# Performance work log

Measured on AMD Instinct MI355X. Metric: run time of the kernel, lower is better.

## Reference

```python
import jax, jax.numpy as jnp
import numpy as np

B, SQ, D = 4, 2048, 1536
HEADS, KV_HEADS, HEAD_DIM = 24, 12, 64
CROSS_DIM = 768
TEXT_LEN, NUM_TOKENS = 512, 64
ENC_LEN = TEXT_LEN + NUM_TOKENS
ROT_DIM = 32
IP_SCALE = 1.0
SCALE = 1.0 / np.sqrt(HEAD_DIM).astype(np.float32)


def _split_heads(x, n_heads):
    # [B, S, n_heads*HEAD_DIM] -> [B, n_heads, S, HEAD_DIM]
    b, s, _ = x.shape
    return x.reshape(b, s, n_heads, HEAD_DIM).transpose(0, 2, 1, 3)


def _repeat_kv(x):
    # [B, KV_HEADS, S, D] -> [B, HEADS, S, D] (repeat_interleave on head dim)
    return jnp.repeat(x, HEADS // KV_HEADS, axis=1)


def _apply_rope(x, cos, sin):
    # x: [B, H, S, ROT_DIM]; cos/sin: [S, ROT_DIM]; use_real_unbind_dim=-2 convention
    xr = x.reshape(*x.shape[:-1], 2, ROT_DIM // 2)
    x_real, x_imag = xr[..., 0, :], xr[..., 1, :]
    x_rot = jnp.concatenate([-x_imag, x_real], axis=-1)
    return x * cos[None, None] + x_rot * sin[None, None]


def _attn(q, k, v):
    scores = jnp.einsum('bhqd,bhkd->bhqk', q, k) * SCALE
    probs = jax.nn.softmax(scores.astype(jnp.float32), axis=-1).astype(q.dtype)
    return jnp.einsum('bhqk,bhkd->bhqd', probs, v)


def setup_inputs():
    key = jax.random.key(0)
    ks = jax.random.split(key, 10)
    t = jnp.arange(SQ, dtype=jnp.float32)
    freqs = 1.0 / (10000.0 ** (jnp.arange(ROT_DIM // 2, dtype=jnp.float32) / (ROT_DIM // 2)))
    ang = t[:, None] * freqs[None, :]  # [SQ, ROT_DIM//2]
    rope_cos = jnp.concatenate([jnp.cos(ang), jnp.cos(ang)], axis=-1)
    rope_sin = jnp.concatenate([jnp.sin(ang), jnp.sin(ang)], axis=-1)
    s = 0.02
    return {
        'hidden_states': jax.random.normal(ks[0], (B, SQ, D), jnp.float32),
        'encoder_hidden_states': jax.random.normal(ks[1], (B, ENC_LEN, CROSS_DIM), jnp.float32),
        'rope_cos': rope_cos,
        'rope_sin': rope_sin,
        'wq': jax.random.normal(ks[2], (D, HEADS * HEAD_DIM), jnp.float32) * s,
        'wk': jax.random.normal(ks[3], (CROSS_DIM, KV_HEADS * HEAD_DIM), jnp.float32) * s,
        'wv': jax.random.normal(ks[4], (CROSS_DIM, KV_HEADS * HEAD_DIM), jnp.float32) * s,
        'wk_ip': jax.random.normal(ks[5], (CROSS_DIM, KV_HEADS * HEAD_DIM), jnp.float32) * s,
        'wv_ip': jax.random.normal(ks[6], (CROSS_DIM, KV_HEADS * HEAD_DIM), jnp.float32) * s,
        'wo': jax.random.normal(ks[7], (HEADS * HEAD_DIM, D), jnp.float32) * s,
        'bo': jnp.zeros((D,), jnp.float32),
    }


def reference(hidden_states, encoder_hidden_states, rope_cos, rope_sin,
              wq, wk, wv, wk_ip, wv_ip, wo, bo):
    residual = hidden_states
    text = encoder_hidden_states[:, :TEXT_LEN, :]
    ip = encoder_hidden_states[:, TEXT_LEN:, :]

    q = _split_heads(hidden_states @ wq, HEADS)          # [B, H, SQ, Dh]
    k = _repeat_kv(_split_heads(text @ wk, KV_HEADS))    # [B, H, St, Dh]
    v = _repeat_kv(_split_heads(text @ wv, KV_HEADS))

    # RoPE in float32 on first ROT_DIM channels of Q only (cross-attention)
    q32 = q.astype(jnp.float32)
    q_rot = _apply_rope(q32[..., :ROT_DIM], rope_cos, rope_sin)
    q = jnp.concatenate([q_rot, q32[..., ROT_DIM:]], axis=-1).astype(hidden_states.dtype)

    out = _attn(q, k, v)                                 # [B, H, SQ, Dh]

    # IP-adapter branch
    ip_k = _repeat_kv(_split_heads(ip @ wk_ip, KV_HEADS))  # [B, H, NUM_TOKENS, Dh]
    ip_v = _repeat_kv(_split_heads(ip @ wv_ip, KV_HEADS))
    out = out + IP_SCALE * _attn(q, ip_k, ip_v)

    out = out.transpose(0, 2, 1, 3).reshape(B, SQ, HEADS * HEAD_DIM)
    out = out @ wo + bo
    return out + residual
```

## Files before the change

### kernel.cpp

```cpp
#include <hip/hip_runtime.h>
#include <hip/hip_bf16.h>

typedef __attribute__((ext_vector_type(8))) short short8;
typedef __attribute__((ext_vector_type(4))) short short4v;
typedef __attribute__((ext_vector_type(4))) float f32x4;

#define MFMA16(a, b, c) __builtin_amdgcn_mfma_f32_16x16x32_bf16(a, b, c, 0, 0, 0)
#define QK_SCALE_LOG2E 0.18033688011112042f

__device__ __forceinline__ short f2bf(float x) {
  union { float f; unsigned u; } v; v.f = x;
  unsigned u = v.u;
  u += 0x7FFFu + ((u >> 16) & 1u);
  return (short)(u >> 16);
}
__device__ __forceinline__ short f2bf_trunc(float x) {
  union { float f; unsigned u; } v; v.f = x;
  return (short)(v.u >> 16);
}

__device__ __forceinline__ void gload16(const void* g, void* l) {
  __builtin_amdgcn_global_load_lds(
      (const __attribute__((address_space(1))) unsigned int*)g,
      (__attribute__((address_space(3))) unsigned int*)l, 16, 0, 0);
}

__global__ __launch_bounds__(256) void enc_pack_kernel(
    const float* __restrict__ enc, short* __restrict__ text,
    short* __restrict__ ip) {
  int i4 = blockIdx.x * 256 + threadIdx.x;
  int i = i4 * 4;
  if (i >= 4 * 576 * 768) return;
  int c = i % 768;
  int rs = i / 768;
  int b = rs / 576, s = rs % 576;
  f32x4 v = *(const f32x4*)(enc + i);
  short4v o;
  o[0] = f2bf(v[0]); o[1] = f2bf(v[1]); o[2] = f2bf(v[2]); o[3] = f2bf(v[3]);
  if (s < 512)
    *(short4v*)(text + (size_t)(b * 512 + s) * 768 + c) = o;
  else
    *(short4v*)(ip + (size_t)(b * 64 + (s - 512)) * 768 + c) = o;
}

__global__ __launch_bounds__(256) void prep_weights_kernel(
    const float* __restrict__ wq, const float* __restrict__ wo,
    const float* __restrict__ wk, const float* __restrict__ wv,
    const float* __restrict__ wkip, const float* __restrict__ wvip,
    short* __restrict__ wqT, short* __restrict__ woT,
    short* __restrict__ wkvT, short* __restrict__ wkvipT) {
  __shared__ float tile[32][33];
  const int z = blockIdx.z;
  const float* src; short* dst; int N, row_off;
  if (z == 0)      { src = wq;   dst = wqT;    N = 1536; row_off = 0; }
  else if (z == 1) { src = wo;   dst = woT;    N = 1536; row_off = 0; }
  else if (z == 2) { src = wk;   dst = wkvT;   N = 768;  row_off = 0; }
  else if (z == 3) { src = wv;   dst = wkvT;   N = 768;  row_off = 768; }
  else if (z == 4) { src = wkip; dst = wkvipT; N = 768;  row_off = 0; }
  else             { src = wvip; dst = wkvipT; N = 768;  row_off = 768; }
  int c0 = blockIdx.x * 32, r0 = blockIdx.y * 32;
  if (c0 >= N || r0 >= N) return;
  int tx = threadIdx.x & 31, ty = threadIdx.x >> 5;
#pragma unroll
  for (int j = 0; j < 4; ++j)
    tile[ty + j * 8][tx] = src[(size_t)(r0 + ty + j * 8) * N + c0 + tx];
  __syncthreads();
#pragma unroll
  for (int j = 0; j < 4; ++j)
    dst[(size_t)(row_off + c0 + ty + j * 8) * N + r0 + tx] =
        f2bf(tile[tx][ty + j * 8]);
}

__device__ __forceinline__ void stage32(const short* __restrict__ gA,
                                        const short* __restrict__ gBt,
                                        int lda, int ldb, char* buf, int tid) {
#pragma unroll
  for (int li = 0; li < 2; ++li) {
    int L = li * 4096 + tid * 16;
    int row = L >> 6;
    int cb = (L & 63) ^ (((row >> 1) & 3) << 4);
    gload16(gA + (size_t)row * lda + (cb >> 1), buf + L);
    gload16(gBt + (size_t)row * ldb + (cb >> 1), buf + 8192 + L);
  }
}

__device__ __forceinline__ void compute32(const char* p0, int wr, int wc,
                                          int lr, int hk, int xr,
                                          f32x4 acc[4][4]) {
  short8 af[4], bf[4];
#pragma unroll
  for (int m = 0; m < 4; ++m) {
    int row = wr + m * 16 + lr;
    af[m] = *(const short8*)(p0 + row * 64 + (hk ^ xr));
  }
#pragma unroll
  for (int n = 0; n < 4; ++n) {
    int row = wc + n * 16 + lr;
    bf[n] = *(const short8*)(p0 + 8192 + row * 64 + (hk ^ xr));
  }
#pragma unroll
  for (int m = 0; m < 4; ++m)
#pragma unroll
    for (int n = 0; n < 4; ++n) acc[m][n] = MFMA16(af[m], bf[n], acc[m][n]);
}

template <int K>
__device__ __forceinline__ void gemm128p(
    const short* __restrict__ A, const short* __restrict__ Bt, int lda,
    int ldb, int row0, int col0, char* sm, f32x4 acc[4][4]) {
  const int tid = threadIdx.x;
  const int lane = tid & 63, wid = tid >> 6;
  const int wr = (wid >> 1) * 64, wc = (wid & 1) * 64;
  const int lr = lane & 15;
  const int hk = (lane >> 4) * 16;
  const int xr = ((lr >> 1) & 3) << 4;
  constexpr int NT = K / 32;

  const short* gA = A + (size_t)row0 * lda;
  const short* gB = Bt + (size_t)col0 * ldb;

  char* p0 = sm;
  char* p1 = sm + 16384;
  char* p2 = sm + 32768;

  stage32(gA, gB, lda, ldb, p0, tid);
  stage32(gA + 32, gB + 32, lda, ldb, p1, tid);
  asm volatile("s_waitcnt vmcnt(4)" ::: "memory");
  __builtin_amdgcn_s_barrier();

  for (int t = 0; t < NT; ++t) {
    if (t + 2 < NT)
      stage32(gA + (t + 2) * 32, gB + (t + 2) * 32, lda, ldb, p2, tid);
    __builtin_amdgcn_sched_barrier(0);
    compute32(p0, wr, wc, lr, hk, xr, acc);
    __builtin_amdgcn_sched_barrier(0);
    if (t + 2 < NT)
      asm volatile("s_waitcnt vmcnt(4)" ::: "memory");
    else
      asm volatile("s_waitcnt vmcnt(0)" ::: "memory");
    __builtin_amdgcn_s_barrier();
    char* tmp = p0; p0 = p1; p1 = p2; p2 = tmp;
  }
}

__device__ __forceinline__ void grid128(int& row0, int& col0) {
  int bid = blockIdx.x;
  int x = bid & 7;
  int j = bid >> 3;
  row0 = (x * 8 + (j & 7)) * 128;
  col0 = (j >> 3) * 128;
}

__device__ __forceinline__ void q_issueA(const float* __restrict__ gAf,
                                         int tid, f32x4 ar[4]) {
#pragma unroll
  for (int li = 0; li < 2; ++li) {
    int L = li * 4096 + tid * 16;
    int row = L >> 6;
    int cb = (L & 63) ^ (((row >> 1) & 3) << 4);
    const float* src = gAf + (size_t)row * 1536 + (cb >> 1);
    ar[li * 2] = *(const f32x4*)src;
    ar[li * 2 + 1] = *(const f32x4*)(src + 4);
  }
}
__device__ __forceinline__ void q_writeA(char* buf, int tid, const f32x4 ar[4]) {
#pragma unroll
  for (int li = 0; li < 2; ++li) {
    int L = li * 4096 + tid * 16;
    short8 s;
#pragma unroll
    for (int j = 0; j < 4; ++j) {
      s[j] = f2bf_trunc(ar[li * 2][j]);
      s[j + 4] = f2bf_trunc(ar[li * 2 + 1][j]);
    }
    *(short8*)(buf + L) = s;
  }
}
__device__ __forceinline__ void q_stageB(const short* __restrict__ gBt,
                                         char* buf, int tid) {
#pragma unroll
  for (int li = 0; li < 2; ++li) {
    int L = li * 4096 + tid * 16;
    int row = L >> 6;
    int cb = (L & 63) ^ (((row >> 1) & 3) << 4);
    gload16(gBt + (size_t)row * 1536 + (cb >> 1), buf + 8192 + L);
  }
}

__global__ __launch_bounds__(256, 3) void q_proj_128p(
    const float* __restrict__ hs, const short* __restrict__ wqT,
    const float* __restrict__ rc, const float* __restrict__ rsn,
    short* __restrict__ qbuf) {
  __shared__ char sm[49152];
  f32x4 acc[4][4] = {};
  int row0, col0;
  grid128(row0, col0);

  const int tid = threadIdx.x;
  const int lane = tid & 63, wid = tid >> 6;
  const int wr = (wid >> 1) * 64, wc = (wid & 1) * 64;
  const int lr = lane & 15;
  const int hk = (lane >> 4) * 16;
  const int xr = ((lr >> 1) & 3) << 4;
  constexpr int NT = 48;

  const float* gAf = hs + (size_t)row0 * 1536;
  const short* gB = wqT + (size_t)col0 * 1536;
  char* p0 = sm;
  char* p1 = sm + 16384;
  char* p2 = sm + 32768;
  f32x4 arA[4], arB[4];

  q_issueA(gAf, tid, arA);
  q_stageB(gB, p0, tid);
  q_issueA(gAf + 32, tid, arB);
  q_stageB(gB + 32, p1, tid);
  asm volatile("s_waitcnt vmcnt(8)" ::: "memory");
  q_writeA(p0, tid, arA);
  asm volatile("s_waitcnt vmcnt(6) lgkmcnt(0)" ::: "memory");
  __builtin_amdgcn_s_barrier();

  for (int t = 0; t < NT; ++t) {
    if (t + 2 < NT) {
      if ((t & 1) == 0) q_issueA(gAf + (t + 2) * 32, tid, arA);
      else              q_issueA(gAf + (t + 2) * 32, tid, arB);
      q_stageB(gB + (t + 2) * 32, p2, tid);
    }
    __builtin_amdgcn_sched_barrier(0);
    compute32(p0, wr, wc, lr, hk, xr, acc);
    __builtin_amdgcn_sched_barrier(0);
    if (t + 2 < NT)
      asm volatile("s_waitcnt vmcnt(6)" ::: "memory");
    else
      asm volatile("s_waitcnt vmcnt(0)" ::: "memory");
    if (t + 1 < NT) {
      if ((t & 1) == 0) q_writeA(p1, tid, arB);
      else              q_writeA(p1, tid, arA);
    }
    asm volatile("s_waitcnt lgkmcnt(0)" ::: "memory");
    __builtin_amdgcn_s_barrier();
    char* tmp = p0; p0 = p1; p1 = p2; p2 = tmp;
  }

  const int lrow4 = (lane >> 4) * 4;
  const int h = (col0 + wc) >> 6;
#pragma unroll
  for (int m = 0; m < 4; ++m) {
#pragma unroll
    for (int r = 0; r < 4; ++r) {
      int grow = row0 + wr + m * 16 + lrow4 + r;
      int b = grow >> 11, t = grow & 2047;
      float v0 = acc[m][0][r], v1 = acc[m][1][r];
      float c0 = rc[t * 32 + lr], s0 = rsn[t * 32 + lr];
      float c1 = rc[t * 32 + 16 + lr], s1 = rsn[t * 32 + 16 + lr];
      float n0 = (v0 * c0 - v1 * s0) * QK_SCALE_LOG2E;
      float n1 = (v1 * c1 + v0 * s1) * QK_SCALE_LOG2E;
      short* ob = qbuf + ((size_t)(b * 24 + h) * 2048 + t) * 64;
      ob[lr] = f2bf(n0);
      ob[16 + lr] = f2bf(n1);
      ob[32 + lr] = f2bf(acc[m][2][r] * QK_SCALE_LOG2E);
      ob[48 + lr] = f2bf(acc[m][3][r] * QK_SCALE_LOG2E);
    }
  }
}

__global__ __launch_bounds__(256, 3) void o_proj_128p(
    const short* __restrict__ attnbf, const short* __restrict__ woT,
    const float* __restrict__ bo, const float* __restrict__ resid,
    float* __restrict__ out) {
  __shared__ char sm[49152];
  f32x4 acc[4][4] = {};
  int row0, col0;
  grid128(row0, col0);

  const int tid = threadIdx.x;
  const int lane = tid & 63, wid = tid >> 6;
  const int wr = (wid >> 1) * 64, wc = (wid & 1) * 64;
  const int lr = lane & 15;
  const int hk = (lane >> 4) * 16;
  const int xr = ((lr >> 1) & 3) << 4;
  const int lrow4 = (lane >> 4) * 4;
  constexpr int NT = 48;

  const short* gA = attnbf + (size_t)row0 * 1536;
  const short* gB = woT + (size_t)col0 * 1536;
  char* p0 = sm;
  char* p1 = sm + 16384;
  char* p2 = sm + 32768;
  float rv[2][4][4];

  stage32(gA, gB, 1536, 1536, p0, tid);
  stage32(gA + 32, gB + 32, 1536, 1536, p1, tid);
  asm volatile("s_waitcnt vmcnt(4)" ::: "memory");
  __builtin_amdgcn_s_barrier();

  for (int t = 0; t < NT; ++t) {
    if (t + 2 < NT)
      stage32(gA + (t + 2) * 32, gB + (t + 2) * 32, 1536, 1536, p2, tid);
    if (t == NT - 2) {
#pragma unroll
      for (int m = 0; m < 2; ++m)
#pragma unroll
        for (int n = 0; n < 4; ++n)
#pragma unroll
          for (int r = 0; r < 4; ++r)
            rv[m][n][r] = resid[(size_t)(row0 + wr + m * 16 + lrow4 + r) * 1536 +
                                col0 + wc + n * 16 + lr];
    }
    __builtin_amdgcn_sched_barrier(0);
    compute32(p0, wr, wc, lr, hk, xr, acc);
    __builtin_amdgcn_sched_barrier(0);
    if (t + 2 < NT)
      asm volatile("s_waitcnt vmcnt(4)" ::: "memory");
    else if (t == NT - 2)
      asm volatile("s_waitcnt vmcnt(32)" ::: "memory");
    __builtin_amdgcn_s_barrier();
    char* tmp = p0; p0 = p1; p1 = p2; p2 = tmp;
  }

#pragma unroll
  for (int m = 0; m < 4; ++m) {
#pragma unroll
    for (int n = 0; n < 4; ++n) {
#pragma unroll
      for (int r = 0; r < 4; ++r) {
        int grow = row0 + wr + m * 16 + lrow4 + r;
        int gcol = col0 + wc + n * 16 + lr;
        size_t off = (size_t)grow * 1536 + gcol;
        float rs = (m < 2) ? rv[m & 1][n][r] : resid[off];
        out[off] = acc[m][n][r] + bo[gcol] + rs;
      }
    }
  }
}

__global__ __launch_bounds__(256, 3) void kv_gemm(
    const short* __restrict__ Abf, const short* __restrict__ wkvT,
    short* __restrict__ kout, short* __restrict__ vtout, int rlog2) {
  __shared__ char sm[49152];
  f32x4 acc[4][4] = {};
  const int row0 = blockIdx.y * 128, col0 = blockIdx.x * 128;
  gemm128p<768>(Abf, wkvT, 768, 768, row0, col0, sm, acc);

  const int tid = threadIdx.x;
  const int lane = tid & 63, wid = tid >> 6;
  const int wr = (wid >> 1) * 64, wc = (wid & 1) * 64;
  const int lr = lane & 15, lrow4 = (lane >> 4) * 4;
  const int rmask = (1 << rlog2) - 1;
#pragma unroll
  for (int m = 0; m < 4; ++m) {
#pragma unroll
    for (int n = 0; n < 4; ++n) {
#pragma unroll
      for (int r = 0; r < 4; ++r) {
        int grow = row0 + wr + m * 16 + lrow4 + r;
        int gcol = col0 + wc + n * 16 + lr;
        int b = grow >> rlog2, key = grow & rmask;
        short val = f2bf(acc[m][n][r]);
        if (gcol < 768) {
          int kvh = gcol >> 6, d = gcol & 63;
          kout[((((size_t)(b * 12 + kvh)) << rlog2) + key) * 64 + d] = val;
        } else {
          int c2 = gcol - 768;
          int kvh = c2 >> 6, d = c2 & 63;
          int kp = (key & ~31) | (((key >> 2) & 3) << 3) |
                   (((key >> 4) & 1) << 2) | (key & 3);
          vtout[(((size_t)((b * 12 + kvh) * 64 + d)) << rlog2) + kp] = val;
        }
      }
    }
  }
}

__device__ __forceinline__ void stage_tile(const short* __restrict__ ks,
                                           const short* __restrict__ vs,
                                           int vstr, short* kb, short* vb,
                                           int tid) {
#pragma unroll
  for (int q = 0; q < 2; ++q) {
    int L = q * 4096 + tid * 16;
    int row = L >> 7;
    int sc = ((L & 127) ^ ((row & 7) << 4)) >> 1;
    gload16(ks + row * 64 + sc, (char*)kb + L);
    gload16(vs + (size_t)row * vstr + sc, (char*)vb + L);
  }
}

__device__ __forceinline__ void attn_tile(const short* kb, const short* vb,
                                          const short8 qf[2],
                                          float& m_run, float& l_run,
                                          f32x4 o_acc[4], int lane) {
  const int lr = lane & 15, hi = lane >> 4;
  f32x4 s[4];
#pragma unroll
  for (int nf = 0; nf < 4; ++nf) {
    int row = nf * 16 + lr;
    int rx = (row & 7) << 4;
    const char* base = (const char*)kb + row * 128;
    short8 k0 = *(const short8*)(base + ((hi * 16) ^ rx));
    short8 k1 = *(const short8*)(base + ((64 + hi * 16) ^ rx));
    f32x4 a = {0.f, 0.f, 0.f, 0.f};
    a = MFMA16(k0, qf[0], a);
    a = MFMA16(k1, qf[1], a);
    s[nf] = a;
  }
  float mx = fmaxf(fmaxf(s[0][0], s[0][1]), fmaxf(s[0][2], s[0][3]));
#pragma unroll
  for (int nf = 1; nf < 4; ++nf)
    mx = fmaxf(mx, fmaxf(fmaxf(s[nf][0], s[nf][1]), fmaxf(s[nf][2], s[nf][3])));
  if (__any(mx - m_run > 8.0f)) {
    float mr = fmaxf(mx, __shfl_xor(mx, 16));
    mr = fmaxf(mr, __shfl_xor(mr, 32));
    float mn = fmaxf(m_run, mr);
    float corr = __builtin_amdgcn_exp2f(m_run - mn);
    m_run = mn;
    l_run *= corr;
#pragma unroll
    for (int r = 0; r < 4; ++r) {
      float cr = __shfl(corr, hi * 4 + r);
#pragma unroll
      for (int no = 0; no < 4; ++no) o_acc[no][r] *= cr;
    }
  }
  short8 pa[2];
#pragma unroll
  for (int nf = 0; nf < 4; ++nf) {
#pragma unroll
    for (int r = 0; r < 4; ++r) {
      float p = __builtin_amdgcn_exp2f(s[nf][r] - m_run);
      l_run += p;
      pa[nf >> 1][(nf & 1) * 4 + r] = f2bf_trunc(p);
    }
  }
#pragma unroll
  for (int ks = 0; ks < 2; ++ks) {
#pragma unroll
    for (int no = 0; no < 4; ++no) {
      int row = no * 16 + lr;
      int rx = (row & 7) << 4;
      short8 vf = *(const short8*)((const char*)vb + row * 128 +
                                   ((ks * 64 + hi * 16) ^ rx));
      o_acc[no] = MFMA16(pa[ks], vf, o_acc[no]);
    }
  }
}

__global__ __launch_bounds__(256, 4) void attn_kernel(
    const short* __restrict__ qbuf, const short* __restrict__ kbuf,
    const short* __restrict__ vtbuf, const short* __restrict__ kipbuf,
    const short* __restrict__ vtipbuf, short* __restrict__ attn_out) {
  const int tid = threadIdx.x;
  const int lane = tid & 63, wid = tid >> 6;
  const int f = (blockIdx.x & 7) * 384 + (blockIdx.x >> 3);
  const int qt = f & 31;
  const int h = (f >> 5) % 24;
  const int b = f / (32 * 24);
  const int kvh = h >> 1;
  const int lr = lane & 15, hi = lane >> 4;

  __shared__ short skv_k[2 * 64 * 64];
  __shared__ short skv_v[2 * 64 * 64];

  const short* qp = qbuf + (size_t)(b * 24 + h) * 2048 * 64;
  const short* kp = kbuf + (size_t)(b * 12 + kvh) * 512 * 64;
  const short* vp = vtbuf + (size_t)(b * 12 + kvh) * 64 * 512;
  const short* kip = kipbuf + (size_t)(b * 12 + kvh) * 64 * 64;
  const short* vip = vtipbuf + (size_t)(b * 12 + kvh) * 64 * 64;

  const int q0 = qt * 64 + wid * 16;
  short8 qf[2];
  qf[0] = *(const short8*)(qp + (size_t)(q0 + lr) * 64 + hi * 8);
  qf[1] = *(const short8*)(qp + (size_t)(q0 + lr) * 64 + 32 + hi * 8);

  float m1 = -1.0e30f, l1 = 0.f, m2 = -1.0e30f, l2 = 0.f;
  f32x4 oacc1[4] = {}, oacc2[4] = {};

  stage_tile(kp, vp, 512, skv_k, skv_v, tid);
  __syncthreads();

  for (int t = 0; t < 9; ++t) {
    int cur = t & 1, nxt = cur ^ 1;
    if (t < 8) {
      const short* ks_ = (t < 7) ? kp + (t + 1) * 64 * 64 : kip;
      const short* vs_ = (t < 7) ? vp + (t + 1) * 64 : vip;
      int vstr = (t < 7) ? 512 : 64;
      stage_tile(ks_, vs_, vstr, skv_k + nxt * 4096, skv_v + nxt * 4096, tid);
    }
    if (t < 8)
      attn_tile(skv_k + cur * 4096, skv_v + cur * 4096, qf, m1, l1, oacc1, lane);
    else
      attn_tile(skv_k + cur * 4096, skv_v + cur * 4096, qf, m2, l2, oacc2, lane);
    __syncthreads();
  }

  l1 += __shfl_xor(l1, 16); l1 += __shfl_xor(l1, 32);
  l2 += __shfl_xor(l2, 16); l2 += __shfl_xor(l2, 32);
  float inv1 = 1.0f / l1, inv2 = 1.0f / l2;
#pragma unroll
  for (int r = 0; r < 4; ++r) {
    float i1 = __shfl(inv1, hi * 4 + r);
    float i2 = __shfl(inv2, hi * 4 + r);
    int grow = b * 2048 + q0 + hi * 4 + r;
#pragma unroll
    for (int no = 0; no < 4; ++no) {
      float val = oacc1[no][r] * i1 + oacc2[no][r] * i2;
      attn_out[(size_t)grow * 1536 + h * 64 + no * 16 + lr] = f2bf(val);
    }
  }
}

extern "C" void kernel_launch(void* const* d_in, const int* in_sizes, int n_in,
                              void* d_out, int out_size, void* d_ws, size_t ws_size,
                              hipStream_t stream) {
  const float* hs = (const float*)d_in[0];
  const float* enc = (const float*)d_in[1];
  const float* rc = (const float*)d_in[2];
  const float* rsn = (const float*)d_in[3];
  const float* wq = (const float*)d_in[4];
  const float* wk = (const float*)d_in[5];
  const float* wv = (const float*)d_in[6];
  const float* wkip = (const float*)d_in[7];
  const float* wvip = (const float*)d_in[8];
  const float* wo = (const float*)d_in[9];
  const float* bo = (const float*)d_in[10];
  float* out = (float*)d_out;

  char* ws = (char*)d_ws;
  short* attnbuf = (short*)(ws + 0);
  short* qbuf    = (short*)(ws + 25165824);
  short* kbuf    = (short*)(ws + 50331648);
  short* vtbuf   = (short*)(ws + 53477376);
  short* kipbuf  = (short*)(ws + 56623104);
  short* vtipbuf = (short*)(ws + 57016320);
  short* textbf  = (short*)(ws + 57409536);
  short* ipbf    = (short*)(ws + 60555264);
  short* wqT     = (short*)(ws + 60948480);
  short* woT     = (short*)(ws + 65667072);
  short* wkvT    = (short*)(ws + 70385664);
  short* wkvipT  = (short*)(ws + 72744960);

  enc_pack_kernel<<<1728, 256, 0, stream>>>(enc, textbf, ipbf);
  prep_weights_kernel<<<dim3(48, 48, 6), 256, 0, stream>>>(
      wq, wo, wk, wv, wkip, wvip, wqT, woT, wkvT, wkvipT);

  q_proj_128p<<<768, 256, 0, stream>>>(hs, wqT, rc, rsn, qbuf);
  kv_gemm<<<dim3(12, 16), 256, 0, stream>>>(textbf, wkvT, kbuf, vtbuf, 9);
  kv_gemm<<<dim3(12, 2), 256, 0, stream>>>(ipbf, wkvipT, kipbuf, vtipbuf, 6);

  attn_kernel<<<3072, 256, 0, stream>>>(qbuf, kbuf, vtbuf, kipbuf,
                                        vtipbuf, attnbuf);

  o_proj_128p<<<768, 256, 0, stream>>>(attnbuf, woT, bo, hs, out);
}
```

Baseline: 212.3 us.

## Pre-pack Wo into MFMA fragment order and load B operand directly to registers

The weight prep kernel now writes Wo in a packed layout matching the MFMA B-fragment per lane, so the output projection loads B fragments straight from global memory into double-buffered registers instead of staging them through LDS. This halves shared memory use per block and removes B-side LDS reads and writes, which may raise occupancy. The early prefetch of part of the residual is dropped in favour of plain loads in the epilogue. The cost is more global loads per wave, since each wave pair re-reads its B fragments with no LDS sharing, and latency hiding now depends on the register double buffer.

After: 439.8 us. 2.07x slower.

```diff
diff --git a/kernel.cpp b/kernel.cpp
--- a/kernel.cpp
+++ b/kernel.cpp
@@ -47,13 +47,13 @@
     const float* __restrict__ wq, const float* __restrict__ wo,
     const float* __restrict__ wk, const float* __restrict__ wv,
     const float* __restrict__ wkip, const float* __restrict__ wvip,
-    short* __restrict__ wqT, short* __restrict__ woT,
+    short* __restrict__ wqT, short* __restrict__ woPK,
     short* __restrict__ wkvT, short* __restrict__ wkvipT) {
   __shared__ float tile[32][33];
   const int z = blockIdx.z;
   const float* src; short* dst; int N, row_off;
   if (z == 0)      { src = wq;   dst = wqT;    N = 1536; row_off = 0; }
-  else if (z == 1) { src = wo;   dst = woT;    N = 1536; row_off = 0; }
+  else if (z == 1) { src = wo;   dst = woPK;   N = 1536; row_off = 0; }
   else if (z == 2) { src = wk;   dst = wkvT;   N = 768;  row_off = 0; }
   else if (z == 3) { src = wv;   dst = wkvT;   N = 768;  row_off = 768; }
   else if (z == 4) { src = wkip; dst = wkvipT; N = 768;  row_off = 0; }
@@ -65,10 +65,21 @@
   for (int j = 0; j < 4; ++j)
     tile[ty + j * 8][tx] = src[(size_t)(r0 + ty + j * 8) * N + c0 + tx];
   __syncthreads();
-#pragma unroll
-  for (int j = 0; j < 4; ++j)
-    dst[(size_t)(row_off + c0 + ty + j * 8) * N + r0 + tx] =
-        f2bf(tile[tx][ty + j * 8]);
+  if (z == 1) {
+#pragma unroll
+    for (int j = 0; j < 4; ++j) {
+      int n = c0 + ty + j * 8;
+      int k = r0 + tx;
+      size_t idx = ((size_t)((n >> 4) * 48 + (k >> 5)) * 64 +
+                    (((k >> 3) & 3) << 4) + (n & 15)) * 8 + (k & 7);
+      dst[idx] = f2bf(tile[tx][ty + j * 8]);
+    }
+  } else {
+#pragma unroll
+    for (int j = 0; j < 4; ++j)
+      dst[(size_t)(row_off + c0 + ty + j * 8) * N + r0 + tx] =
+          f2bf(tile[tx][ty + j * 8]);
+  }
 }
 
 __device__ __forceinline__ void stage32(const short* __restrict__ gA,
@@ -141,6 +152,33 @@
     __builtin_amdgcn_s_barrier();
     char* tmp = p0; p0 = p1; p1 = p2; p2 = tmp;
   }
+}
+
+__device__ __forceinline__ void stageA32(const short* __restrict__ gA,
+                                         char* buf, int tid) {
+#pragma unroll
+  for (int li = 0; li < 2; ++li) {
+    int L = li * 4096 + tid * 16;
+    int row = L >> 6;
+    int cb = (L & 63) ^ (((row >> 1) & 3) << 4);
+    gload16(gA + (size_t)row * 1536 + (cb >> 1), buf + L);
+  }
+}
+
+__device__ __forceinline__ void compute32A(const char* p, int wr, int lr,
+                                           int hk, int xr,
+                                           const short8 bf[4],
+                                           f32x4 acc[4][4]) {
+  short8 af[4];
+#pragma unroll
+  for (int m = 0; m < 4; ++m) {
+    int row = wr + m * 16 + lr;
+    af[m] = *(const short8*)(p + row * 64 + (hk ^ xr));
+  }
+#pragma unroll
+  for (int m = 0; m < 4; ++m)
+#pragma unroll
+    for (int n = 0; n < 4; ++n) acc[m][n] = MFMA16(af[m], bf[n], acc[m][n]);
 }
 
 __device__ __forceinline__ void grid128(int& row0, int& col0) {
@@ -264,11 +302,11 @@
   }
 }
 
-__global__ __launch_bounds__(256, 3) void o_proj_128p(
-    const short* __restrict__ attnbf, const short* __restrict__ woT,
+__global__ __launch_bounds__(256, 3) void o_proj_128B(
+    const short* __restrict__ attnbf, const short* __restrict__ woPK,
     const float* __restrict__ bo, const float* __restrict__ resid,
     float* __restrict__ out) {
-  __shared__ char sm[49152];
+  __shared__ char sm[24576];
   f32x4 acc[4][4] = {};
   int row0, col0;
   grid128(row0, col0);
@@ -279,45 +317,54 @@
   const int lr = lane & 15;
   const int hk = (lane >> 4) * 16;
   const int xr = ((lr >> 1) & 3) << 4;
-  const int lrow4 = (lane >> 4) * 4;
   constexpr int NT = 48;
 
   const short* gA = attnbf + (size_t)row0 * 1536;
-  const short* gB = woT + (size_t)col0 * 1536;
+  const short* bq = woPK +
+      ((size_t)(((col0 >> 4) + ((wid & 1) << 2)) * 48) * 64 + lane) * 8;
+  short8 bfA[4], bfB[4];
+
   char* p0 = sm;
-  char* p1 = sm + 16384;
-  char* p2 = sm + 32768;
-  float rv[2][4][4];
-
-  stage32(gA, gB, 1536, 1536, p0, tid);
-  stage32(gA + 32, gB + 32, 1536, 1536, p1, tid);
+  char* p1 = sm + 8192;
+  char* p2 = sm + 16384;
+
+  stageA32(gA, p0, tid);
+  stageA32(gA + 32, p1, tid);
+#pragma unroll
+  for (int n = 0; n < 4; ++n)
+    bfA[n] = *(const short8*)(bq + (size_t)(n * 48) * 512);
   asm volatile("s_waitcnt vmcnt(4)" ::: "memory");
   __builtin_amdgcn_s_barrier();
 
   for (int t = 0; t < NT; ++t) {
-    if (t + 2 < NT)
-      stage32(gA + (t + 2) * 32, gB + (t + 2) * 32, 1536, 1536, p2, tid);
-    if (t == NT - 2) {
-#pragma unroll
-      for (int m = 0; m < 2; ++m)
+    if (t + 2 < NT) stageA32(gA + (t + 2) * 32, p2, tid);
+    if (t + 1 < NT) {
+      if ((t & 1) == 0) {
 #pragma unroll
         for (int n = 0; n < 4; ++n)
-#pragma unroll
-          for (int r = 0; r < 4; ++r)
-            rv[m][n][r] = resid[(size_t)(row0 + wr + m * 16 + lrow4 + r) * 1536 +
-                                col0 + wc + n * 16 + lr];
-    }
-    __builtin_amdgcn_sched_barrier(0);
-    compute32(p0, wr, wc, lr, hk, xr, acc);
+          bfB[n] = *(const short8*)(bq + (size_t)(n * 48 + t + 1) * 512);
+      } else {
+#pragma unroll
+        for (int n = 0; n < 4; ++n)
+          bfA[n] = *(const short8*)(bq + (size_t)(n * 48 + t + 1) * 512);
+      }
+    }
     __builtin_amdgcn_sched_barrier(0);
     if (t + 2 < NT)
+      asm volatile("s_waitcnt vmcnt(6)" ::: "memory");
+    else if (t + 1 < NT)
       asm volatile("s_waitcnt vmcnt(4)" ::: "memory");
-    else if (t == NT - 2)
-      asm volatile("s_waitcnt vmcnt(32)" ::: "memory");
+    else
+      asm volatile("s_waitcnt vmcnt(0)" ::: "memory");
+    __builtin_amdgcn_sched_barrier(0);
+    if ((t & 1) == 0) compute32A(p0, wr, lr, hk, xr, bfA, acc);
+    else              compute32A(p0, wr, lr, hk, xr, bfB, acc);
+    __builtin_amdgcn_sched_barrier(0);
     __builtin_amdgcn_s_barrier();
     char* tmp = p0; p0 = p1; p1 = p2; p2 = tmp;
   }
 
+  const int lrow4 = (lane >> 4) * 4;
 #pragma unroll
   for (int m = 0; m < 4; ++m) {
 #pragma unroll
@@ -327,8 +374,7 @@
         int grow = row0 + wr + m * 16 + lrow4 + r;
         int gcol = col0 + wc + n * 16 + lr;
         size_t off = (size_t)grow * 1536 + gcol;
-        float rs = (m < 2) ? rv[m & 1][n][r] : resid[off];
-        out[off] = acc[m][n][r] + bo[gcol] + rs;
+        out[off] = acc[m][n][r] + bo[gcol] + resid[off];
       }
     }
   }
@@ -535,13 +581,13 @@
   short* textbf  = (short*)(ws + 57409536);
   short* ipbf    = (short*)(ws + 60555264);
   short* wqT     = (short*)(ws + 60948480);
-  short* woT     = (short*)(ws + 65667072);
+  short* woPK    = (short*)(ws + 65667072);
   short* wkvT    = (short*)(ws + 70385664);
   short* wkvipT  = (short*)(ws + 72744960);
 
   enc_pack_kernel<<<1728, 256, 0, stream>>>(enc, textbf, ipbf);
   prep_weights_kernel<<<dim3(48, 48, 6), 256, 0, stream>>>(
-      wq, wo, wk, wv, wkip, wvip, wqT, woT, wkvT, wkvipT);
+      wq, wo, wk, wv, wkip, wvip, wqT, woPK, wkvT, wkvipT);
 
   q_proj_128p<<<768, 256, 0, stream>>>(hs, wqT, rc, rsn, qbuf);
   kv_gemm<<<dim3(12, 16), 256, 0, stream>>>(textbf, wkvT, kbuf, vtbuf, 9);
@@ -550,5 +596,5 @@
   attn_kernel<<<3072, 256, 0, stream>>>(qbuf, kbuf, vtbuf, kipbuf,
                                         vtipbuf, attnbuf);
 
-  o_proj_128p<<<768, 256, 0, stream>>>(attnbuf, woT, bo, hs, out);
-}
+  o_proj_128B<<<768, 256, 0, stream>>>(attnbuf, woPK, bo, hs, out);
+}
```
